# Performance work log

Measured on AMD Instinct MI355X. Metric: run time of the kernel, lower is better.

Reference implementation:

```python
import jax, jax.numpy as jnp
import numpy as np

TAU = 0.07
EPS = 1e-12  # matches torch F.normalize default eps


def setup_inputs() -> dict:
    key = jax.random.key(0)
    k1, k2 = jax.random.split(key)
    B, C, H, W, K = 4, 256, 256, 256, 19
    feat = jax.random.normal(k1, (B, C, H, W), dtype=jnp.float32)
    # binary ground-truth one-hot-ish masks; gt.eq(1) selects positives
    gt = jax.random.randint(k2, (B, K, H, W), 0, 2).astype(jnp.float32)
    return {"feat": feat, "gt": gt}


def _l2norm(x, axis):
    n = jnp.sqrt(jnp.sum(x * x, axis=axis, keepdims=True))
    return x / jnp.maximum(n, EPS)


def reference(feat, gt):
    # feat: [B,C,H,W], gt: [B,K,H,W] binary
    pos = (gt == 1.0).astype(feat.dtype)              # [B,K,H,W]
    fnorm = _l2norm(feat, axis=1)                     # per-pixel L2 normalize over C
    # scatter-add normalized features into class prototypes
    k0 = jnp.einsum('bkhw,bchw->kc', pos, fnorm)      # [K,C]
    k0n = _l2norm(k0, axis=1)                         # [K,C]
    # prototype-vs-pixel similarities, softmax over classes
    logits = jnp.einsum('kc,bchw->bkhw', k0n, fnorm) / TAU  # [B,K,H,W]
    logp = jax.nn.log_softmax(logits, axis=1)
    num_pos = jnp.sum(pos)
    loss = -jnp.sum(pos * logp) / num_pos
    return loss
```

## Files before the change

kernel.cpp:

```cpp
#include <hip/hip_runtime.h>
#include <math.h>

namespace {
constexpr int Cn = 256;
constexpr int Kn = 19;
constexpr int HW = 256 * 256;
constexpr int P  = 4 * HW;
constexpr float TAUv = 0.07f;
constexpr float EPSv = 1e-12f;

constexpr int K0_OFF   = 0;
constexpr int K0N_OFF  = 4864;
constexpr int SUMS_OFF = 9728;
constexpr int ZERO_N   = 9730;
constexpr int P1_GRID  = 1024;
constexpr int P3_GRID  = P / 256;
}

__global__ __launch_bounds__(256) void gc_init(float* __restrict__ ws) {
  int i = blockIdx.x * 256 + threadIdx.x;
  if (i < ZERO_N) ws[i] = 0.0f;
}

__global__ __launch_bounds__(256, 4) void gc_phase1(const float* __restrict__ feat,
                                                    const float* __restrict__ gt,
                                                    float* __restrict__ k0) {
  __shared__ float tile[32 * 256];
  __shared__ float part[256];
  __shared__ float wls[32][20];

  const int t = threadIdx.x;
  const int p = t & 31;
  const int g = t >> 5;

  float acc[Kn];
#pragma unroll
  for (int k = 0; k < Kn; k++) acc[k] = 0.0f;

  for (int tid = blockIdx.x; tid < P / 32; tid += gridDim.x) {
    const int p0  = tid << 5;
    const int b   = p0 >> 16;
    const int hw0 = p0 & (HW - 1);
    const float* fb = feat + (size_t)b * (Cn * HW) + hw0;

    __syncthreads();

    float v[32];
#pragma unroll
    for (int j = 0; j < 32; j++) v[j] = fb[(size_t)((g << 5) + j) * HW + p];
    float ss = 0.0f;
#pragma unroll
    for (int j = 0; j < 32; j++) {
      const int c = (g << 5) + j;
      ss += v[j] * v[j];
      tile[(p << 8) + (c ^ p)] = v[j];
    }
    part[t] = ss;

    unsigned msk = 0;
    if (t < 32) {
      const float* gb = gt + (size_t)b * (Kn * HW) + hw0 + p;
#pragma unroll
      for (int k = 0; k < Kn; k++)
        msk |= (gb[(size_t)k * HW] == 1.0f) ? (1u << k) : 0u;
    }

    __syncthreads();

    if (t < 32) {
      float fss = 0.0f;
#pragma unroll
      for (int q = 0; q < 8; q++) fss += part[(q << 5) + p];
      const float rn = 1.0f / fmaxf(sqrtf(fss), EPSv);
#pragma unroll
      for (int k = 0; k < Kn; k++) wls[p][k] = ((msk >> k) & 1u) ? rn : 0.0f;
      wls[p][19] = 0.0f;
    }

    __syncthreads();

#pragma unroll 4
    for (int pp = 0; pp < 32; pp++) {
      const float4 w0 = *(const float4*)&wls[pp][0];
      const float4 w1 = *(const float4*)&wls[pp][4];
      const float4 w2 = *(const float4*)&wls[pp][8];
      const float4 w3 = *(const float4*)&wls[pp][12];
      const float4 w4 = *(const float4*)&wls[pp][16];
      const float fv = tile[(pp << 8) + (t ^ pp)];
      acc[0]  = fmaf(fv, w0.x, acc[0]);  acc[1]  = fmaf(fv, w0.y, acc[1]);
      acc[2]  = fmaf(fv, w0.z, acc[2]);  acc[3]  = fmaf(fv, w0.w, acc[3]);
      acc[4]  = fmaf(fv, w1.x, acc[4]);  acc[5]  = fmaf(fv, w1.y, acc[5]);
      acc[6]  = fmaf(fv, w1.z, acc[6]);  acc[7]  = fmaf(fv, w1.w, acc[7]);
      acc[8]  = fmaf(fv, w2.x, acc[8]);  acc[9]  = fmaf(fv, w2.y, acc[9]);
      acc[10] = fmaf(fv, w2.z, acc[10]); acc[11] = fmaf(fv, w2.w, acc[11]);
      acc[12] = fmaf(fv, w3.x, acc[12]); acc[13] = fmaf(fv, w3.y, acc[13]);
      acc[14] = fmaf(fv, w3.z, acc[14]); acc[15] = fmaf(fv, w3.w, acc[15]);
      acc[16] = fmaf(fv, w4.x, acc[16]); acc[17] = fmaf(fv, w4.y, acc[17]);
      acc[18] = fmaf(fv, w4.z, acc[18]);
    }
  }

#pragma unroll
  for (int k = 0; k < Kn; k++) atomicAdd(&k0[k * 256 + t], acc[k]);
}

__global__ __launch_bounds__(256) void gc_phase2(const float* __restrict__ k0,
                                                 float* __restrict__ k0n) {
  const int lane = threadIdx.x & 63;
  const int wv   = threadIdx.x >> 6;
  for (int r = wv; r < Kn; r += 4) {
    float s = 0.0f;
#pragma unroll
    for (int j = 0; j < 4; j++) {
      const float v = k0[r * 256 + (j << 6) + lane];
      s += v * v;
    }
#pragma unroll
    for (int off = 32; off > 0; off >>= 1) s += __shfl_down(s, off);
    s = __shfl(s, 0);
    const float rn = 1.0f / fmaxf(sqrtf(s), EPSv);
#pragma unroll
    for (int j = 0; j < 4; j++) {
      const int c = (j << 6) + lane;
      k0n[r * 256 + c] = k0[r * 256 + c] * rn;
    }
  }
}

__global__ __launch_bounds__(256, 4) void gc_phase3(const float* __restrict__ feat,
                                                    const float* __restrict__ gt,
                                                    const float* __restrict__ k0n,
                                                    float* __restrict__ sums) {
  __shared__ float wco[Kn * 256];
  __shared__ float tile[16 * 256];

  const int t = threadIdx.x;
#pragma unroll
  for (int i = 0; i < Kn; i++) wco[i * 256 + t] = k0n[i * 256 + t];

  const int pix0 = blockIdx.x << 8;
  const int b    = pix0 >> 16;
  const int hw   = (pix0 & (HW - 1)) + t;
  const float* fb = feat + (size_t)b * (Cn * HW) + hw;

  float dot[Kn];
#pragma unroll
  for (int k = 0; k < Kn; k++) dot[k] = 0.0f;
  float ss = 0.0f;

  float v[16];
#pragma unroll
  for (int j = 0; j < 16; j++) v[j] = fb[(size_t)j * HW];

  for (int c0 = 0; c0 < Cn; c0 += 16) {
    __syncthreads();
#pragma unroll
    for (int j = 0; j < 16; j++) tile[j * 256 + t] = v[j];
    __syncthreads();

    if (c0 + 16 < Cn) {
#pragma unroll
      for (int j = 0; j < 16; j++) v[j] = fb[(size_t)(c0 + 16 + j) * HW];
    }

#pragma unroll
    for (int j4 = 0; j4 < 16; j4 += 4) {
      const float f0 = tile[(j4 + 0) * 256 + t];
      const float f1 = tile[(j4 + 1) * 256 + t];
      const float f2 = tile[(j4 + 2) * 256 + t];
      const float f3 = tile[(j4 + 3) * 256 + t];
      ss = fmaf(f0, f0, ss); ss = fmaf(f1, f1, ss);
      ss = fmaf(f2, f2, ss); ss = fmaf(f3, f3, ss);
#pragma unroll
      for (int k = 0; k < Kn; k++) {
        const float4 w = *(const float4*)&wco[k * 256 + c0 + j4];
        dot[k] = fmaf(f3, w.w, fmaf(f2, w.z, fmaf(f1, w.y, fmaf(f0, w.x, dot[k]))));
      }
    }
  }

  const float sc = 1.0f / (fmaxf(sqrtf(ss), EPSv) * TAUv);
  float mx = -1e30f;
#pragma unroll
  for (int k = 0; k < Kn; k++) { dot[k] *= sc; mx = fmaxf(mx, dot[k]); }
  float se = 0.0f;
#pragma unroll
  for (int k = 0; k < Kn; k++) se += __expf(dot[k] - mx);
  const float lse = __logf(se) + mx;

  const float* gb = gt + (size_t)b * (Kn * HW) + hw;
  float lsum = 0.0f, npos = 0.0f;
#pragma unroll
  for (int k = 0; k < Kn; k++) {
    if (gb[(size_t)k * HW] == 1.0f) { lsum += lse - dot[k]; npos += 1.0f; }
  }

#pragma unroll
  for (int off = 32; off > 0; off >>= 1) {
    lsum += __shfl_down(lsum, off);
    npos += __shfl_down(npos, off);
  }
  if ((t & 63) == 0) {
    atomicAdd(&sums[0], lsum);
    atomicAdd(&sums[1], npos);
  }
}

__global__ void gc_finalize(const float* __restrict__ sums, float* __restrict__ out) {
  if (threadIdx.x == 0 && blockIdx.x == 0)
    out[0] = sums[0] / sums[1];
}

extern "C" void kernel_launch(void* const* d_in, const int* in_sizes, int n_in,
                              void* d_out, int out_size, void* d_ws, size_t ws_size,
                              hipStream_t stream) {
  const float* feat = (const float*)d_in[0];
  const float* gt   = (const float*)d_in[1];
  float* ws  = (float*)d_ws;
  float* out = (float*)d_out;

  float* k0   = ws + K0_OFF;
  float* k0n  = ws + K0N_OFF;
  float* sums = ws + SUMS_OFF;

  gc_init<<<dim3((ZERO_N + 255) / 256), dim3(256), 0, stream>>>(ws);
  gc_phase1<<<dim3(P1_GRID), dim3(256), 0, stream>>>(feat, gt, k0);
  gc_phase2<<<dim3(1), dim3(256), 0, stream>>>(k0, k0n);
  gc_phase3<<<dim3(P3_GRID), dim3(256), 0, stream>>>(feat, gt, k0n, sums);
  gc_finalize<<<dim3(1), dim3(64), 0, stream>>>(sums, out);
}
```

Baseline: 603.8 us.

## Use scalar-broadcast masks in phase1 and register double-buffering with global weights in phase3

Phase1 now stores one inverse norm and one class bitmask per pixel in shared memory instead of a 32x20 weight table. These values are broadcast to scalar registers with readfirstlane, and each weight is selected per class from the bitmask, which removes five LDS float4 loads per pixel. Phase3 drops the shared-memory staging of both the feature tile and the prototype matrix. It double-buffers feature loads in registers and reads the prototypes directly from global memory with uniform addresses, which removes the barriers and LDS traffic. The trade-off is more registers and per-iteration global or scalar loads of the prototypes, which rely on the cache instead of LDS.

```diff
diff --git a/kernel.cpp b/kernel.cpp
--- a/kernel.cpp
+++ b/kernel.cpp
@@ -17,6 +17,13 @@
 constexpr int P3_GRID  = P / 256;
 }
 
+__device__ __forceinline__ float bcast_f(float x) {
+  return __uint_as_float((unsigned)__builtin_amdgcn_readfirstlane((int)__float_as_uint(x)));
+}
+__device__ __forceinline__ unsigned bcast_u(unsigned x) {
+  return (unsigned)__builtin_amdgcn_readfirstlane((int)x);
+}
+
 __global__ __launch_bounds__(256) void gc_init(float* __restrict__ ws) {
   int i = blockIdx.x * 256 + threadIdx.x;
   if (i < ZERO_N) ws[i] = 0.0f;
@@ -27,7 +34,8 @@
                                                     float* __restrict__ k0) {
   __shared__ float tile[32 * 256];
   __shared__ float part[256];
-  __shared__ float wls[32][20];
+  __shared__ float rnL[32];
+  __shared__ unsigned mskL[32];
 
   const int t = threadIdx.x;
   const int p = t & 31;
@@ -71,32 +79,22 @@
       float fss = 0.0f;
 #pragma unroll
       for (int q = 0; q < 8; q++) fss += part[(q << 5) + p];
-      const float rn = 1.0f / fmaxf(sqrtf(fss), EPSv);
-#pragma unroll
-      for (int k = 0; k < Kn; k++) wls[p][k] = ((msk >> k) & 1u) ? rn : 0.0f;
-      wls[p][19] = 0.0f;
+      rnL[p]  = 1.0f / fmaxf(sqrtf(fss), EPSv);
+      mskL[p] = msk;
     }
 
     __syncthreads();
 
-#pragma unroll 4
+#pragma unroll 8
     for (int pp = 0; pp < 32; pp++) {
-      const float4 w0 = *(const float4*)&wls[pp][0];
-      const float4 w1 = *(const float4*)&wls[pp][4];
-      const float4 w2 = *(const float4*)&wls[pp][8];
-      const float4 w3 = *(const float4*)&wls[pp][12];
-      const float4 w4 = *(const float4*)&wls[pp][16];
-      const float fv = tile[(pp << 8) + (t ^ pp)];
-      acc[0]  = fmaf(fv, w0.x, acc[0]);  acc[1]  = fmaf(fv, w0.y, acc[1]);
-      acc[2]  = fmaf(fv, w0.z, acc[2]);  acc[3]  = fmaf(fv, w0.w, acc[3]);
-      acc[4]  = fmaf(fv, w1.x, acc[4]);  acc[5]  = fmaf(fv, w1.y, acc[5]);
-      acc[6]  = fmaf(fv, w1.z, acc[6]);  acc[7]  = fmaf(fv, w1.w, acc[7]);
-      acc[8]  = fmaf(fv, w2.x, acc[8]);  acc[9]  = fmaf(fv, w2.y, acc[9]);
-      acc[10] = fmaf(fv, w2.z, acc[10]); acc[11] = fmaf(fv, w2.w, acc[11]);
-      acc[12] = fmaf(fv, w3.x, acc[12]); acc[13] = fmaf(fv, w3.y, acc[13]);
-      acc[14] = fmaf(fv, w3.z, acc[14]); acc[15] = fmaf(fv, w3.w, acc[15]);
-      acc[16] = fmaf(fv, w4.x, acc[16]); acc[17] = fmaf(fv, w4.y, acc[17]);
-      acc[18] = fmaf(fv, w4.z, acc[18]);
+      const float    rn = bcast_f(rnL[pp]);
+      const unsigned mk = bcast_u(mskL[pp]);
+      const float    fv = tile[(pp << 8) + (t ^ pp)];
+#pragma unroll
+      for (int k = 0; k < Kn; k++) {
+        const float w = ((mk >> k) & 1u) ? rn : 0.0f;
+        acc[k] = fmaf(fv, w, acc[k]);
+      }
     }
   }
 
@@ -127,17 +125,34 @@
   }
 }
 
+__device__ __forceinline__ void p3_load(float (&dst)[16],
+                                        const float* __restrict__ fb, int base) {
+#pragma unroll
+  for (int j = 0; j < 16; j++) dst[j] = fb[(size_t)(base + j) * HW];
+}
+
+__device__ __forceinline__ void p3_compute(const float (&v)[16], int c0,
+                                           const float* __restrict__ k0n,
+                                           float (&dot)[Kn], float& ss) {
+#pragma unroll
+  for (int j4 = 0; j4 < 16; j4 += 4) {
+    const float f0 = v[j4 + 0], f1 = v[j4 + 1];
+    const float f2 = v[j4 + 2], f3 = v[j4 + 3];
+    ss = fmaf(f0, f0, ss); ss = fmaf(f1, f1, ss);
+    ss = fmaf(f2, f2, ss); ss = fmaf(f3, f3, ss);
+#pragma unroll
+    for (int k = 0; k < Kn; k++) {
+      const float4 w = *(const float4*)(k0n + k * 256 + c0 + j4);
+      dot[k] = fmaf(f3, w.w, fmaf(f2, w.z, fmaf(f1, w.y, fmaf(f0, w.x, dot[k]))));
+    }
+  }
+}
+
 __global__ __launch_bounds__(256, 4) void gc_phase3(const float* __restrict__ feat,
                                                     const float* __restrict__ gt,
                                                     const float* __restrict__ k0n,
                                                     float* __restrict__ sums) {
-  __shared__ float wco[Kn * 256];
-  __shared__ float tile[16 * 256];
-
-  const int t = threadIdx.x;
-#pragma unroll
-  for (int i = 0; i < Kn; i++) wco[i * 256 + t] = k0n[i * 256 + t];
-
+  const int t    = threadIdx.x;
   const int pix0 = blockIdx.x << 8;
   const int b    = pix0 >> 16;
   const int hw   = (pix0 & (HW - 1)) + t;
@@ -148,35 +163,13 @@
   for (int k = 0; k < Kn; k++) dot[k] = 0.0f;
   float ss = 0.0f;
 
-  float v[16];
-#pragma unroll
-  for (int j = 0; j < 16; j++) v[j] = fb[(size_t)j * HW];
-
-  for (int c0 = 0; c0 < Cn; c0 += 16) {
-    __syncthreads();
-#pragma unroll
-    for (int j = 0; j < 16; j++) tile[j * 256 + t] = v[j];
-    __syncthreads();
-
-    if (c0 + 16 < Cn) {
-#pragma unroll
-      for (int j = 0; j < 16; j++) v[j] = fb[(size_t)(c0 + 16 + j) * HW];
-    }
-
-#pragma unroll
-    for (int j4 = 0; j4 < 16; j4 += 4) {
-      const float f0 = tile[(j4 + 0) * 256 + t];
-      const float f1 = tile[(j4 + 1) * 256 + t];
-      const float f2 = tile[(j4 + 2) * 256 + t];
-      const float f3 = tile[(j4 + 3) * 256 + t];
-      ss = fmaf(f0, f0, ss); ss = fmaf(f1, f1, ss);
-      ss = fmaf(f2, f2, ss); ss = fmaf(f3, f3, ss);
-#pragma unroll
-      for (int k = 0; k < Kn; k++) {
-        const float4 w = *(const float4*)&wco[k * 256 + c0 + j4];
-        dot[k] = fmaf(f3, w.w, fmaf(f2, w.z, fmaf(f1, w.y, fmaf(f0, w.x, dot[k]))));
-      }
-    }
+  float va[16], vb[16];
+  p3_load(va, fb, 0);
+  for (int c0 = 0; c0 < Cn; c0 += 32) {
+    p3_load(vb, fb, c0 + 16);
+    p3_compute(va, c0, k0n, dot, ss);
+    if (c0 + 32 < Cn) p3_load(va, fb, c0 + 32);
+    p3_compute(vb, c0 + 16, k0n, dot, ss);
   }
 
   const float sc = 1.0f / (fmaxf(sqrtf(ss), EPSv) * TAUv);
```

New measurement: 634.0 us. 1.05x slower.
